# Optimization experiments

Hardware: AMD Instinct MI355X
Metric: run time of the kernel (lower is better)

The kernel has to match this reference:

```python
import jax, jax.numpy as jnp
import numpy as np

N_NODES = 50000
N_EDGES = 800000
D_IN = 128
HEADS = 8
UNITS = 16


def setup_inputs() -> dict:
    key = jax.random.key(0)
    ks = jax.random.split(key, 6)
    x = jax.random.normal(ks[0], (N_NODES, D_IN), dtype=jnp.float32)
    edges = jax.random.randint(ks[1], (N_EDGES, 2), 0, N_NODES, dtype=jnp.int32)
    # glorot_uniform-style init for kernels
    lim_k = float(np.sqrt(6.0 / (D_IN + HEADS * UNITS)))
    kernel = jax.random.uniform(ks[2], (D_IN, HEADS, UNITS), minval=-lim_k, maxval=lim_k, dtype=jnp.float32)
    lim_a = float(np.sqrt(6.0 / (1 + HEADS * UNITS)))
    kernel_attention1 = jax.random.uniform(ks[3], (1, HEADS, UNITS), minval=-lim_a, maxval=lim_a, dtype=jnp.float32)
    bias_attention = jnp.zeros((1, HEADS, UNITS), dtype=jnp.float32)
    bias = jnp.zeros((HEADS * UNITS,), dtype=jnp.float32)
    return {"x": x, "edges": edges, "kernel": kernel,
            "kernel_attention1": kernel_attention1,
            "bias_attention": bias_attention, "bias": bias}


def reference(x, edges, kernel, kernel_attention1, bias_attention, bias):
    # GATv2 (version=2), merge_type='concat', use_bias=True, training=False
    n_nodes = x.shape[0]
    sources = edges[:, 0]
    targets = edges[:, 1]

    xp = jnp.einsum('nd,dhu->nhu', x, kernel)          # [N, H, U]
    xbias = xp + bias_attention                        # [N, H, U]

    # per-edge attention score: leaky_relu(x_t + x_s) . a   (GATv2)
    s = jax.nn.leaky_relu(xbias[targets] + xbias[sources], negative_slope=0.2)  # [E, H, U]
    scores = jnp.sum(s * kernel_attention1, axis=-1)   # [E, H]

    # segment softmax over incoming edges of each target node
    smax = jax.ops.segment_max(scores, targets, num_segments=n_nodes)  # [N, H]
    scores = jnp.exp(scores - smax[targets])
    ssum = jax.ops.segment_sum(scores, targets, num_segments=n_nodes)  # [N, H]
    scores = scores / (ssum[targets] + 1e-7)           # [E, H]

    # weighted scatter-aggregate of source features
    out = jax.ops.segment_sum(scores[..., None] * xp[sources], targets,
                              num_segments=n_nodes)    # [N, H, U]
    out = out.reshape(n_nodes, HEADS * UNITS) + bias   # concat heads
    return jax.nn.gelu(out, approximate=True)
```

## Files before the change

### kernel.cpp

```cpp
#include <hip/hip_runtime.h>
#include <hip/hip_fp16.h>


#define CAP   64
#define CAPB  56
#define SB    256
#define NBH   98

__device__ __forceinline__ uint2 pack_half4(float4 v) {
    __half2 a = __floats2half2_rn(v.x, v.y);
    __half2 b = __floats2half2_rn(v.z, v.w);
    uint2 r;
    r.x = *(unsigned int*)&a;
    r.y = *(unsigned int*)&b;
    return r;
}

__device__ __forceinline__ float4 unpack_half4(uint2 r) {
    __half2 a = *(__half2*)&r.x;
    __half2 b = *(__half2*)&r.y;
    const float2 fa = __half22float2(a);
    const float2 fb = __half22float2(b);
    return make_float4(fa.x, fa.y, fb.x, fb.y);
}

__device__ __forceinline__ float gelu_tanh(float x) {
    const float y = 0.7978845608028654f * fmaf(0.044715f * x, x * x, x);
    const float e = __expf(2.f * y);
    const float th = 1.f - 2.f / (e + 1.f);
    return 0.5f * x * (1.f + th);
}


__global__ __launch_bounds__(256) void gemm_bucket(
    const float* __restrict__ x, const float* __restrict__ w,
    const int* __restrict__ edges,
    unsigned short* __restrict__ xph,
    unsigned int* __restrict__ bkt, int* __restrict__ bbc,
    int N, int E, int gemmB, int nbuck) {
    __shared__ float xl[64 * 129];
    const int tid = threadIdx.x;
    const int bid = blockIdx.x;

    if (bid < gemmB) {
        const int rb = bid << 6;
        const float4* x4 = (const float4*)x;
        for (int i = tid; i < 64 * 32; i += 256) {
            const int r = i >> 5, c = i & 31;
            const int row = rb + r;
            float4 v = make_float4(0.f, 0.f, 0.f, 0.f);
            if (row < N) v = x4[(size_t)row * 32 + c];
            float* dst = &xl[r * 129 + c * 4];
            dst[0] = v.x; dst[1] = v.y; dst[2] = v.z; dst[3] = v.w;
        }
        __syncthreads();

        const int lane = tid & 63;
        const int wv = __builtin_amdgcn_readfirstlane(tid >> 6);
        const int cb = wv << 5;

        float4 acc[8];
#pragma unroll
        for (int j = 0; j < 8; ++j) acc[j] = make_float4(0.f, 0.f, 0.f, 0.f);

        const float* xrow = &xl[lane * 129];
#pragma unroll 2
        for (int k = 0; k < 128; ++k) {
            const float xv = xrow[k];
            const float4* wr = (const float4*)(w + (k << 7) + cb);
#pragma unroll
            for (int j = 0; j < 8; ++j) {
                const float4 wvv = wr[j];
                acc[j].x = fmaf(xv, wvv.x, acc[j].x);
                acc[j].y = fmaf(xv, wvv.y, acc[j].y);
                acc[j].z = fmaf(xv, wvv.z, acc[j].z);
                acc[j].w = fmaf(xv, wvv.w, acc[j].w);
            }
        }

        const int row = rb + lane;
        if (row < N) {
            uint2* o = (uint2*)(xph + (size_t)row * 128 + cb);
#pragma unroll
            for (int j = 0; j < 8; ++j) o[j] = pack_half4(acc[j]);
        }
    } else {
        const int sb = bid - gemmB;
        unsigned int* eb = (unsigned int*)xl;
        int* hist = (int*)xl + NBH * CAPB;
        const int chunk = (E + SB - 1) / SB;
        const int e0 = sb * chunk;
        const int e1 = min(E, e0 + chunk);
        const int2* __restrict__ e2 = (const int2*)edges;

        for (int h = 0; h < 2; ++h) {
            if (tid < NBH) hist[tid] = 0;
            __syncthreads();
            const int blo = h * NBH;
            for (int i = e0 + tid; i < e1; i += 256) {
                const int2 v = e2[i];
                const int b = v.y >> 8;
                if (b >= blo && b < blo + NBH) {
                    const int lb = b - blo;
                    const int pos = atomicAdd(&hist[lb], 1);
                    eb[lb * CAPB + pos] =
                        ((unsigned int)v.x << 8) | (unsigned int)(v.y & 255);
                }
            }
            __syncthreads();
            const size_t gbase = ((size_t)sb * nbuck + blo) * CAPB;
            for (int i = tid; i < NBH * CAPB; i += 256) bkt[gbase + i] = eb[i];
            if (tid < NBH) bbc[(blo + tid) * SB + sb] = hist[tid];
            __syncthreads();
        }
    }
}


__global__ __launch_bounds__(256) void build_lists(
    const unsigned int* __restrict__ bkt, const int* __restrict__ bbc,
    int* __restrict__ cnt, int* __restrict__ srcs, int N, int nbuck) {
    __shared__ int lst[256 * CAP];
    __shared__ int cl[256];
    __shared__ int cA[SB];
    const int b = blockIdx.x;
    const int tid = threadIdx.x;

    cl[tid] = 0;
    cA[tid] = bbc[b * SB + tid];
    __syncthreads();

    const int wv = tid >> 6, lane = tid & 63;
    for (int k = 0; k < 64; k += 4) {
        int ce[4];
        unsigned int ev[4];
#pragma unroll
        for (int u = 0; u < 4; ++u) {
            const int sb = (wv << 6) + k + u;
            ce[u] = cA[sb];
            ev[u] = (lane < ce[u])
                        ? bkt[((size_t)sb * nbuck + b) * CAPB + lane]
                        : 0u;
        }
#pragma unroll
        for (int u = 0; u < 4; ++u) {
            if (lane < ce[u]) {
                const int ni = ev[u] & 255;
                const int pos = atomicAdd(&cl[ni], 1);
                lst[(ni << 6) + pos] = (int)(ev[u] >> 8);
            }
        }
    }
    __syncthreads();

    const int nb = b << 8;
    if (nb + tid < N) cnt[nb + tid] = cl[tid];
    for (int i = tid; i < 256 * CAP; i += 256) {
        if (nb + (i >> 6) < N) srcs[((size_t)nb << 6) + i] = lst[i];
    }
}


__device__ __forceinline__ void edge_accum4(const float4 xs, const float4 base,
                                            const float4 ka, const float mask,
                                            float4& acc, float& ssum) {
    float a0 = base.x + xs.x; a0 = fmaxf(a0, 0.2f * a0);
    float a1 = base.y + xs.y; a1 = fmaxf(a1, 0.2f * a1);
    float a2 = base.z + xs.z; a2 = fmaxf(a2, 0.2f * a2);
    float a3 = base.w + xs.w; a3 = fmaxf(a3, 0.2f * a3);
    float p = a0 * ka.x;
    p = fmaf(a1, ka.y, p);
    p = fmaf(a2, ka.z, p);
    p = fmaf(a3, ka.w, p);
    p += __shfl_xor(p, 1);
    p += __shfl_xor(p, 2);
    const float esc = __expf(p) * mask;
    acc.x = fmaf(esc, xs.x, acc.x);
    acc.y = fmaf(esc, xs.y, acc.y);
    acc.z = fmaf(esc, xs.z, acc.z);
    acc.w = fmaf(esc, xs.w, acc.w);
    ssum += esc;
}

__global__ __launch_bounds__(256) void gather_pad(
    const unsigned short* __restrict__ xph, const int* __restrict__ cnt,
    const int* __restrict__ srcs, const float* __restrict__ katt,
    const float* __restrict__ batt, const float* __restrict__ bias,
    float* __restrict__ out, int N) {
    const int node = (blockIdx.x * blockDim.x + threadIdx.x) >> 6;
    const int lane = threadIdx.x & 63;
    if (node >= N) return;
    const int c = lane & 31;
    const int half = lane >> 5;

    const int len = cnt[node];
    const int sv = srcs[(node << 6) + lane];

    const uint2* __restrict__ xp4 = (const uint2*)xph;
    const float4 xt = unpack_half4(xp4[(size_t)node * 32 + c]);
    const float4 ka = ((const float4*)katt)[c];
    const float4 ba = ((const float4*)batt)[c];
    float4 base;
    base.x = xt.x + 2.f * ba.x;
    base.y = xt.y + 2.f * ba.y;
    base.z = xt.z + 2.f * ba.z;
    base.w = xt.w + 2.f * ba.w;

    float4 acc = make_float4(0.f, 0.f, 0.f, 0.f);
    float ssum = 0.f;

    int jj = 0;
    for (; jj + 8 <= len; jj += 8) {
        const int s0 = __shfl(sv, jj + half);
        const int s1 = __shfl(sv, jj + 2 + half);
        const int s2 = __shfl(sv, jj + 4 + half);
        const int s3 = __shfl(sv, jj + 6 + half);
        const uint2 r0 = xp4[(size_t)s0 * 32 + c];
        const uint2 r1 = xp4[(size_t)s1 * 32 + c];
        const uint2 r2 = xp4[(size_t)s2 * 32 + c];
        const uint2 r3 = xp4[(size_t)s3 * 32 + c];
        edge_accum4(unpack_half4(r0), base, ka, 1.f, acc, ssum);
        edge_accum4(unpack_half4(r1), base, ka, 1.f, acc, ssum);
        edge_accum4(unpack_half4(r2), base, ka, 1.f, acc, ssum);
        edge_accum4(unpack_half4(r3), base, ka, 1.f, acc, ssum);
    }
    for (; jj + 4 <= len; jj += 4) {
        const int s0 = __shfl(sv, jj + half);
        const int s1 = __shfl(sv, jj + 2 + half);
        const uint2 r0 = xp4[(size_t)s0 * 32 + c];
        const uint2 r1 = xp4[(size_t)s1 * 32 + c];
        edge_accum4(unpack_half4(r0), base, ka, 1.f, acc, ssum);
        edge_accum4(unpack_half4(r1), base, ka, 1.f, acc, ssum);
    }
    for (; jj < len; jj += 2) {
        const int j = jj + half;
        int s = __shfl(sv, j & 63);
        const bool valid = (j < len);
        s = valid ? s : 0;
        const uint2 rr = xp4[(size_t)s * 32 + c];
        edge_accum4(unpack_half4(rr), base, ka, valid ? 1.f : 0.f, acc, ssum);
    }

    acc.x += __shfl_xor(acc.x, 32);
    acc.y += __shfl_xor(acc.y, 32);
    acc.z += __shfl_xor(acc.z, 32);
    acc.w += __shfl_xor(acc.w, 32);
    ssum  += __shfl_xor(ssum, 32);

    if (half == 0) {
        const float inv = 1.f / (ssum + 1e-7f);
        const float4 b = ((const float4*)bias)[c];
        float4 o;
        o.x = gelu_tanh(fmaf(acc.x, inv, b.x));
        o.y = gelu_tanh(fmaf(acc.y, inv, b.y));
        o.z = gelu_tanh(fmaf(acc.z, inv, b.z));
        o.w = gelu_tanh(fmaf(acc.w, inv, b.w));
        ((float4*)out)[(size_t)node * 32 + c] = o;
    }
}


extern "C" void kernel_launch(void* const* d_in, const int* in_sizes, int n_in,
                              void* d_out, int out_size, void* d_ws, size_t ws_size,
                              hipStream_t stream) {
    const float* x    = (const float*)d_in[0];
    const int*   edg  = (const int*)d_in[1];
    const float* kern = (const float*)d_in[2];
    const float* katt = (const float*)d_in[3];
    const float* batt = (const float*)d_in[4];
    const float* bias = (const float*)d_in[5];

    const int N = in_sizes[0] / 128;
    const int E = in_sizes[1] / 2;
    const int nbuck = (N + 255) >> 8;

    float* out = (float*)d_out;
    unsigned short* xph = (unsigned short*)d_ws;
    int* cnt  = (int*)(xph + (size_t)N * 128);
    int* srcs = cnt + N;
    int* bbc  = srcs + (size_t)N * CAP;
    unsigned int* bkt = (unsigned int*)(bbc + (size_t)nbuck * SB);

    const int gemmB = (N + 63) / 64;
    gemm_bucket<<<gemmB + SB, 256, 0, stream>>>(x, kern, edg, xph, bkt, bbc,
                                                N, E, gemmB, nbuck);
    build_lists<<<nbuck, 256, 0, stream>>>(bkt, bbc, cnt, srcs, N, nbuck);
    gather_pad<<<(N * 64 + 255) / 256, 256, 0, stream>>>(xph, cnt, srcs, katt,
                                                         batt, bias, out, N);
}
```

Baseline: 167.0 us.

## Split gather into per-head-pair phases over a strip-major fp16 feature layout

The projected features are now stored as four column strips of 32 halves per node instead of one 128-wide row. The gather runs four phases, one per head pair, so each phase randomly reads only a 64-byte slice per source from a much smaller strip that should stay resident in cache. The bucket buffer is transposed so build_lists reads contiguously, build_lists moves to 512 threads, and source lists become 16-bit. In exchange, cnt and srcs are reread four times, and 16-bit source ids only work while N stays below 65536.

```diff
diff --git a/kernel.cpp b/kernel.cpp
--- a/kernel.cpp
+++ b/kernel.cpp
@@ -3,7 +3,7 @@
 
 
 #define CAP   64
-#define CAPB  56
+#define CAPB  64
 #define SB    256
 #define NBH   98
 
@@ -16,14 +16,6 @@
     return r;
 }
 
-__device__ __forceinline__ float4 unpack_half4(uint2 r) {
-    __half2 a = *(__half2*)&r.x;
-    __half2 b = *(__half2*)&r.y;
-    const float2 fa = __half22float2(a);
-    const float2 fb = __half22float2(b);
-    return make_float4(fa.x, fa.y, fb.x, fb.y);
-}
-
 __device__ __forceinline__ float gelu_tanh(float x) {
     const float y = 0.7978845608028654f * fmaf(0.044715f * x, x * x, x);
     const float e = __expf(2.f * y);
@@ -37,7 +29,7 @@
     const int* __restrict__ edges,
     unsigned short* __restrict__ xph,
     unsigned int* __restrict__ bkt, int* __restrict__ bbc,
-    int N, int E, int gemmB, int nbuck) {
+    int N, int E, int gemmB) {
     __shared__ float xl[64 * 129];
     const int tid = threadIdx.x;
     const int bid = blockIdx.x;
@@ -80,7 +72,7 @@
 
         const int row = rb + lane;
         if (row < N) {
-            uint2* o = (uint2*)(xph + (size_t)row * 128 + cb);
+            uint2* o = (uint2*)(xph + ((size_t)wv * N + row) * 32);
 #pragma unroll
             for (int j = 0; j < 8; ++j) o[j] = pack_half4(acc[j]);
         }
@@ -103,13 +95,15 @@
                 if (b >= blo && b < blo + NBH) {
                     const int lb = b - blo;
                     const int pos = atomicAdd(&hist[lb], 1);
-                    eb[lb * CAPB + pos] =
+                    eb[(lb << 6) + pos] =
                         ((unsigned int)v.x << 8) | (unsigned int)(v.y & 255);
                 }
             }
             __syncthreads();
-            const size_t gbase = ((size_t)sb * nbuck + blo) * CAPB;
-            for (int i = tid; i < NBH * CAPB; i += 256) bkt[gbase + i] = eb[i];
+            for (int i = tid; i < NBH * CAPB; i += 256) {
+                const int lb = i >> 6, off = i & 63;
+                bkt[(((size_t)(blo + lb) * SB + sb) << 6) + off] = eb[i];
+            }
             if (tid < NBH) bbc[(blo + tid) * SB + sb] = hist[tid];
             __syncthreads();
         }
@@ -117,29 +111,31 @@
 }
 
 
-__global__ __launch_bounds__(256) void build_lists(
+__global__ __launch_bounds__(512) void build_lists(
     const unsigned int* __restrict__ bkt, const int* __restrict__ bbc,
-    int* __restrict__ cnt, int* __restrict__ srcs, int N, int nbuck) {
+    int* __restrict__ cnt, unsigned short* __restrict__ srcs, int N) {
     __shared__ int lst[256 * CAP];
     __shared__ int cl[256];
     __shared__ int cA[SB];
     const int b = blockIdx.x;
     const int tid = threadIdx.x;
 
-    cl[tid] = 0;
-    cA[tid] = bbc[b * SB + tid];
+    if (tid < 256) {
+        cl[tid] = 0;
+        cA[tid] = bbc[b * SB + tid];
+    }
     __syncthreads();
 
     const int wv = tid >> 6, lane = tid & 63;
-    for (int k = 0; k < 64; k += 4) {
+    for (int k = 0; k < 32; k += 4) {
         int ce[4];
         unsigned int ev[4];
 #pragma unroll
         for (int u = 0; u < 4; ++u) {
-            const int sb = (wv << 6) + k + u;
+            const int sb = (wv << 5) + k + u;
             ce[u] = cA[sb];
             ev[u] = (lane < ce[u])
-                        ? bkt[((size_t)sb * nbuck + b) * CAPB + lane]
+                        ? bkt[(((size_t)b * SB + sb) << 6) + lane]
                         : 0u;
         }
 #pragma unroll
@@ -154,108 +150,68 @@
     __syncthreads();
 
     const int nb = b << 8;
-    if (nb + tid < N) cnt[nb + tid] = cl[tid];
-    for (int i = tid; i < 256 * CAP; i += 256) {
-        if (nb + (i >> 6) < N) srcs[((size_t)nb << 6) + i] = lst[i];
-    }
-}
-
-
-__device__ __forceinline__ void edge_accum4(const float4 xs, const float4 base,
-                                            const float4 ka, const float mask,
-                                            float4& acc, float& ssum) {
-    float a0 = base.x + xs.x; a0 = fmaxf(a0, 0.2f * a0);
-    float a1 = base.y + xs.y; a1 = fmaxf(a1, 0.2f * a1);
-    float a2 = base.z + xs.z; a2 = fmaxf(a2, 0.2f * a2);
-    float a3 = base.w + xs.w; a3 = fmaxf(a3, 0.2f * a3);
-    float p = a0 * ka.x;
-    p = fmaf(a1, ka.y, p);
-    p = fmaf(a2, ka.z, p);
-    p = fmaf(a3, ka.w, p);
-    p += __shfl_xor(p, 1);
-    p += __shfl_xor(p, 2);
-    const float esc = __expf(p) * mask;
-    acc.x = fmaf(esc, xs.x, acc.x);
-    acc.y = fmaf(esc, xs.y, acc.y);
-    acc.z = fmaf(esc, xs.z, acc.z);
-    acc.w = fmaf(esc, xs.w, acc.w);
-    ssum += esc;
-}
-
-__global__ __launch_bounds__(256) void gather_pad(
+    if (tid < 256 && nb + tid < N) cnt[nb + tid] = cl[tid];
+    for (int i = tid; i < 256 * CAP; i += 512) {
+        if (nb + (i >> 6) < N)
+            srcs[((size_t)nb << 6) + i] = (unsigned short)lst[i];
+    }
+}
+
+
+__global__ __launch_bounds__(256) void gather_phase(
     const unsigned short* __restrict__ xph, const int* __restrict__ cnt,
-    const int* __restrict__ srcs, const float* __restrict__ katt,
+    const unsigned short* __restrict__ srcs, const float* __restrict__ katt,
     const float* __restrict__ batt, const float* __restrict__ bias,
     float* __restrict__ out, int N) {
-    const int node = (blockIdx.x * blockDim.x + threadIdx.x) >> 6;
+    const int pair = blockIdx.x >> 14;
+    const int node = ((blockIdx.x & 16383) << 2) + (threadIdx.x >> 6);
+    if (node >= N) return;
     const int lane = threadIdx.x & 63;
-    if (node >= N) return;
-    const int c = lane & 31;
-    const int half = lane >> 5;
+    const int slot = lane >> 4;
+    const int u    = lane & 15;
+    const int h    = (lane >> 3) & 1;
 
     const int len = cnt[node];
-    const int sv = srcs[(node << 6) + lane];
-
-    const uint2* __restrict__ xp4 = (const uint2*)xph;
-    const float4 xt = unpack_half4(xp4[(size_t)node * 32 + c]);
-    const float4 ka = ((const float4*)katt)[c];
-    const float4 ba = ((const float4*)batt)[c];
-    float4 base;
-    base.x = xt.x + 2.f * ba.x;
-    base.y = xt.y + 2.f * ba.y;
-    base.z = xt.z + 2.f * ba.z;
-    base.w = xt.w + 2.f * ba.w;
-
-    float4 acc = make_float4(0.f, 0.f, 0.f, 0.f);
-    float ssum = 0.f;
-
-    int jj = 0;
-    for (; jj + 8 <= len; jj += 8) {
-        const int s0 = __shfl(sv, jj + half);
-        const int s1 = __shfl(sv, jj + 2 + half);
-        const int s2 = __shfl(sv, jj + 4 + half);
-        const int s3 = __shfl(sv, jj + 6 + half);
-        const uint2 r0 = xp4[(size_t)s0 * 32 + c];
-        const uint2 r1 = xp4[(size_t)s1 * 32 + c];
-        const uint2 r2 = xp4[(size_t)s2 * 32 + c];
-        const uint2 r3 = xp4[(size_t)s3 * 32 + c];
-        edge_accum4(unpack_half4(r0), base, ka, 1.f, acc, ssum);
-        edge_accum4(unpack_half4(r1), base, ka, 1.f, acc, ssum);
-        edge_accum4(unpack_half4(r2), base, ka, 1.f, acc, ssum);
-        edge_accum4(unpack_half4(r3), base, ka, 1.f, acc, ssum);
-    }
-    for (; jj + 4 <= len; jj += 4) {
-        const int s0 = __shfl(sv, jj + half);
-        const int s1 = __shfl(sv, jj + 2 + half);
-        const uint2 r0 = xp4[(size_t)s0 * 32 + c];
-        const uint2 r1 = xp4[(size_t)s1 * 32 + c];
-        edge_accum4(unpack_half4(r0), base, ka, 1.f, acc, ssum);
-        edge_accum4(unpack_half4(r1), base, ka, 1.f, acc, ssum);
-    }
-    for (; jj < len; jj += 2) {
-        const int j = jj + half;
+    const int sv  = srcs[((size_t)node << 6) + lane];
+
+    const unsigned int* __restrict__ xp2 = (const unsigned int*)xph;
+    const size_t strip = (size_t)pair * N;
+
+    const float2 xtf = __half22float2(*(const __half2*)&xp2[(strip + node) * 16 + u]);
+    const float2 ka = ((const float2*)katt)[((pair << 1) + h) * 8 + (u & 7)];
+    const float2 ba = ((const float2*)batt)[((pair << 1) + h) * 8 + (u & 7)];
+    const float bx = xtf.x + 2.f * ba.x;
+    const float by = xtf.y + 2.f * ba.y;
+
+    float ax = 0.f, ay = 0.f, ssum = 0.f;
+    for (int jj = 0; jj < len; jj += 4) {
+        const int j = jj + slot;
+        const bool valid = (j < len);
         int s = __shfl(sv, j & 63);
-        const bool valid = (j < len);
         s = valid ? s : 0;
-        const uint2 rr = xp4[(size_t)s * 32 + c];
-        edge_accum4(unpack_half4(rr), base, ka, valid ? 1.f : 0.f, acc, ssum);
-    }
-
-    acc.x += __shfl_xor(acc.x, 32);
-    acc.y += __shfl_xor(acc.y, 32);
-    acc.z += __shfl_xor(acc.z, 32);
-    acc.w += __shfl_xor(acc.w, 32);
-    ssum  += __shfl_xor(ssum, 32);
-
-    if (half == 0) {
+        const unsigned int r = xp2[(strip + s) * 16 + u];
+        const float2 xs = __half22float2(*(const __half2*)&r);
+        float a0 = bx + xs.x; a0 = fmaxf(a0, 0.2f * a0);
+        float a1 = by + xs.y; a1 = fmaxf(a1, 0.2f * a1);
+        float p = fmaf(a0, ka.x, a1 * ka.y);
+        p += __shfl_xor(p, 1);
+        p += __shfl_xor(p, 2);
+        p += __shfl_xor(p, 4);
+        const float esc = valid ? __expf(p) : 0.f;
+        ax = fmaf(esc, xs.x, ax);
+        ay = fmaf(esc, xs.y, ay);
+        ssum += esc;
+    }
+    ax += __shfl_xor(ax, 16); ay += __shfl_xor(ay, 16); ssum += __shfl_xor(ssum, 16);
+    ax += __shfl_xor(ax, 32); ay += __shfl_xor(ay, 32); ssum += __shfl_xor(ssum, 32);
+
+    if (slot == 0) {
         const float inv = 1.f / (ssum + 1e-7f);
-        const float4 b = ((const float4*)bias)[c];
-        float4 o;
-        o.x = gelu_tanh(fmaf(acc.x, inv, b.x));
-        o.y = gelu_tanh(fmaf(acc.y, inv, b.y));
-        o.z = gelu_tanh(fmaf(acc.z, inv, b.z));
-        o.w = gelu_tanh(fmaf(acc.w, inv, b.w));
-        ((float4*)out)[(size_t)node * 32 + c] = o;
+        const float2 bz = ((const float2*)bias)[(pair << 4) + u];
+        float2 o;
+        o.x = gelu_tanh(fmaf(ax, inv, bz.x));
+        o.y = gelu_tanh(fmaf(ay, inv, bz.y));
+        ((float2*)out)[(size_t)node * 64 + (pair << 4) + u] = o;
     }
 }
 
@@ -276,15 +232,15 @@
 
     float* out = (float*)d_out;
     unsigned short* xph = (unsigned short*)d_ws;
-    int* cnt  = (int*)(xph + (size_t)N * 128);
-    int* srcs = cnt + N;
-    int* bbc  = srcs + (size_t)N * CAP;
+    int* cnt = (int*)(xph + (size_t)N * 128);
+    unsigned short* srcs16 = (unsigned short*)(cnt + N);
+    int* bbc = (int*)(srcs16 + (size_t)N * CAP);
     unsigned int* bkt = (unsigned int*)(bbc + (size_t)nbuck * SB);
 
     const int gemmB = (N + 63) / 64;
     gemm_bucket<<<gemmB + SB, 256, 0, stream>>>(x, kern, edg, xph, bkt, bbc,
-                                                N, E, gemmB, nbuck);
-    build_lists<<<nbuck, 256, 0, stream>>>(bkt, bbc, cnt, srcs, N, nbuck);
-    gather_pad<<<(N * 64 + 255) / 256, 256, 0, stream>>>(xph, cnt, srcs, katt,
-                                                         batt, bias, out, N);
-}
+                                                N, E, gemmB);
+    build_lists<<<nbuck, 512, 0, stream>>>(bkt, bbc, cnt, srcs16, N);
+    gather_phase<<<4 << 14, 256, 0, stream>>>(xph, cnt, srcs16, katt, batt,
+                                              bias, out, N);
+}
```

Measured after the change: 222.2 us. +33.1%, slower.
